# Kernel optimization log

Measured on AMD Instinct MI355X. Metric: run time of the kernel, lower is better.

## Reference

```python
import jax, jax.numpy as jnp
import numpy as np

N_NODES = 100000
N_EDGES = 1600000
NUM_FEAT = 128
HIDDEN = 64
NUM_OUT = 21


def gcn_conv(x, src, dst, norm, W, b, n):
    # PyG GCNConv: h = x @ W (no bias in lin); aggregate normalized messages; add bias.
    h = x @ W  # [N, out]
    msg = h[src] * norm[:, None]  # gather + scale, [E+N, out]
    out = jax.ops.segment_sum(msg, dst, num_segments=n)  # scatter-add, [N, out]
    return out + b


def gcn_norm(edge_index, n, dtype):
    # Add self-loops, compute symmetric normalization deg^-1/2[src]*deg^-1/2[dst].
    loop = jnp.arange(n, dtype=edge_index.dtype)
    src = jnp.concatenate([edge_index[0], loop])
    dst = jnp.concatenate([edge_index[1], loop])
    deg = jax.ops.segment_sum(jnp.ones_like(dst, dtype=dtype), dst, num_segments=n)
    dinv = jnp.where(deg > 0, deg ** -0.5, 0.0).astype(dtype)
    norm = dinv[src] * dinv[dst]
    return src, dst, norm


def setup_inputs() -> dict:
    key = jax.random.key(0)
    k1, k2, k3, k4, k5 = jax.random.split(key, 5)
    x = jax.random.normal(k1, (N_NODES, NUM_FEAT), dtype=jnp.float32)
    edge_index = jax.random.randint(k2, (2, N_EDGES), 0, N_NODES, dtype=jnp.int64)
    s1 = 1.0 / np.sqrt(NUM_FEAT)
    s2 = 1.0 / np.sqrt(HIDDEN)
    W1 = jax.random.uniform(k3, (NUM_FEAT, HIDDEN), jnp.float32, -s1, s1)
    b1 = jnp.zeros((HIDDEN,), jnp.float32)
    W2 = jax.random.uniform(k4, (HIDDEN, NUM_OUT), jnp.float32, -s2, s2)
    b2 = jnp.zeros((NUM_OUT,), jnp.float32)
    return {"x": x, "edge_index": edge_index, "W1": W1, "b1": b1, "W2": W2, "b2": b2}


def reference(x, edge_index, W1, b1, W2, b2):
    n = x.shape[0]
    src, dst, norm = gcn_norm(edge_index, n, x.dtype)
    h = gcn_conv(x, src, dst, norm, W1, b1, n)
    h = jax.nn.relu(h)
    out = gcn_conv(h, src, dst, norm, W2, b2, n)
    return out
```

## Files before the change

### kernel.cpp

```cpp
#include <hip/hip_runtime.h>

#define NFEAT 128
#define NHID  64
#define NOUT  21
#define BSH   7
#define BCAP  8192
#define CHUNK 4096
#define EPT   (CHUNK/256)
#define PADI  16
#define NBUKMAX 1024

typedef unsigned int uint;
typedef unsigned short ushort_t;

typedef __bf16 bf16_t;
typedef bf16_t bf16x8 __attribute__((ext_vector_type(8)));
typedef float  f32x4  __attribute__((ext_vector_type(4)));

__device__ inline uint packbf2(float a, float b) {
    uint ua = __float_as_uint(a), ub = __float_as_uint(b);
    ua = (ua + 0x7FFFu + ((ua >> 16) & 1u)) >> 16;
    ub = (ub + 0x7FFFu + ((ub >> 16) & 1u)) >> 16;
    return ua | (ub << 16);
}
__device__ inline float bflo(uint v) { return __uint_as_float(v << 16); }
__device__ inline float bfhi(uint v) { return __uint_as_float(v & 0xffff0000u); }


__global__ __launch_bounds__(256) void k_lsort(const int* __restrict__ src, const int* __restrict__ dst,
                                               uint* __restrict__ ebuf, int* __restrict__ tab,
                                               int* __restrict__ gcnt, int E, int nbuk) {
    __shared__ int  lcnt[NBUKMAX + 1];
    __shared__ int  lsum[256];
    __shared__ uint lsorted[CHUNK];
    int c = blockIdx.x, tid = threadIdx.x;
    int base = c * CHUNK;
    int ccnt = min(CHUNK, E - base);

    for (int j = tid; j <= nbuk; j += 256) lcnt[j] = 0;
    __syncthreads();

    int  buk[EPT];
    uint rec[EPT];
#pragma unroll
    for (int k = 0; k < EPT; ++k) {
        int e = base + k * 256 + tid;
        if (e < E) {
            int d = dst[e];
            buk[k] = d >> BSH;
            rec[k] = ((uint)(d & ((1 << BSH) - 1)) << 17) | (uint)src[e];
            atomicAdd(&lcnt[buk[k]], 1);
        }
    }
    __syncthreads();

    int g = (nbuk + 255) / 256;
    int j0 = tid * g;
    int s = 0;
    for (int j = 0; j < g; ++j) { int idx = j0 + j; if (idx < nbuk) s += lcnt[idx]; }
    lsum[tid] = s;
    __syncthreads();
    for (int off = 1; off < 256; off <<= 1) {
        int t = (tid >= off) ? lsum[tid - off] : 0;
        __syncthreads();
        lsum[tid] += t;
        __syncthreads();
    }
    int run = lsum[tid] - s;
    for (int j = 0; j < g; ++j) {
        int idx = j0 + j;
        if (idx < nbuk) { int cv = lcnt[idx]; lcnt[idx] = run; run += cv; }
    }
    __syncthreads();
    if (tid == 0) lcnt[nbuk] = ccnt;
    __syncthreads();

    for (int j = tid; j < nbuk; j += 256) {
        int st = lcnt[j];
        tab[(size_t)c * (nbuk + 1) + j] = st;
        int cj = lcnt[j + 1] - st;
        if (cj) atomicAdd(&gcnt[j * PADI], cj);
    }
    if (tid == 0) tab[(size_t)c * (nbuk + 1) + nbuk] = ccnt;
    __syncthreads();

#pragma unroll
    for (int k = 0; k < EPT; ++k) {
        int e = base + k * 256 + tid;
        if (e < E) {
            int pos = atomicAdd(&lcnt[buk[k]], 1);
            lsorted[pos] = rec[k];
        }
    }
    __syncthreads();
    for (int i = tid; i < ccnt; i += 256) ebuf[base + i] = lsorted[i];
}


__global__ __launch_bounds__(256) void k_bscan(const int* __restrict__ gcnt, int* __restrict__ bbase,
                                               int* __restrict__ rowptr, int nbuk, int N, int E) {
    __shared__ int lv[NBUKMAX];
    __shared__ int lsum[256];
    int tid = threadIdx.x;
    int g = (nbuk + 255) / 256;
    int j0 = tid * g;
    int s = 0;
    for (int j = 0; j < g; ++j) {
        int idx = j0 + j;
        int v = (idx < nbuk) ? gcnt[idx * PADI] : 0;
        if (idx < nbuk) lv[idx] = v;
        s += v;
    }
    lsum[tid] = s;
    __syncthreads();
    for (int off = 1; off < 256; off <<= 1) {
        int t = (tid >= off) ? lsum[tid - off] : 0;
        __syncthreads();
        lsum[tid] += t;
        __syncthreads();
    }
    int run = lsum[tid] - s;
    for (int j = 0; j < g; ++j) {
        int idx = j0 + j;
        if (idx < nbuk) { bbase[idx] = run; run += lv[idx]; }
    }
    if (tid == 0) rowptr[N] = E;
}


__global__ __launch_bounds__(256) void k_bsort2(const uint* __restrict__ ebuf, const int* __restrict__ tab,
                                                const int* __restrict__ bbase_, const int* __restrict__ gcnt,
                                                int* __restrict__ rowptr, float* __restrict__ dinv,
                                                int* __restrict__ esrc, int nchunk, int nbuk, int N) {
    __shared__ int  ncnt[128];
    __shared__ int  sc[128];
    __shared__ int  lcur[128];
    __shared__ uint stash[BCAP];
    __shared__ int  lpos;
    int b = blockIdx.x, tid = threadIdx.x;
    int nb0 = b << BSH;
    int bb = bbase_[b];
    int cnt_b = gcnt[b * PADI];
    bool fits = (cnt_b <= BCAP);

    if (tid < 128) ncnt[tid] = 0;
    if (tid == 0) lpos = 0;
    __syncthreads();

    for (int c = tid; c < nchunk; c += 256) {
        const int* trow = tab + (size_t)c * (nbuk + 1);
        int s0 = trow[b], e0 = trow[b + 1];
        int len = e0 - s0;
        if (len <= 0) continue;
        const uint* pb = ebuf + (size_t)c * CHUNK;
        if (fits) {
            int pos = atomicAdd(&lpos, len);
            for (int i = 0; i < len; ++i) {
                uint r = pb[s0 + i];
                stash[pos + i] = r;
                atomicAdd(&ncnt[r >> 17], 1);
            }
        } else {
            for (int i = 0; i < len; ++i) atomicAdd(&ncnt[pb[s0 + i] >> 17], 1);
        }
    }
    __syncthreads();

    int v = (tid < 128) ? ncnt[tid] : 0;
    if (tid < 128) sc[tid] = v;
    __syncthreads();
    for (int off = 1; off < 128; off <<= 1) {
        int t = (tid >= off && tid < 128) ? sc[tid - off] : 0;
        __syncthreads();
        if (tid < 128) sc[tid] += t;
        __syncthreads();
    }
    if (tid < 128) {
        int excl = sc[tid] - v;
        int node = nb0 + tid;
        if (node < N) {
            rowptr[node] = bb + excl;
            dinv[node] = rsqrtf((float)(v + 1));
        }
        lcur[tid] = bb + excl;
    }
    __syncthreads();

    if (fits) {
        for (int i = tid; i < cnt_b; i += 256) {
            uint r = stash[i];
            int pos = atomicAdd(&lcur[r >> 17], 1);
            esrc[pos] = (int)(r & 0x1FFFFu);
        }
    } else {
        for (int c = tid; c < nchunk; c += 256) {
            const int* trow = tab + (size_t)c * (nbuk + 1);
            int s0 = trow[b], e0 = trow[b + 1];
            const uint* pb = ebuf + (size_t)c * CHUNK;
            for (int i = s0; i < e0; ++i) {
                uint r = pb[i];
                int pos = atomicAdd(&lcur[r >> 17], 1);
                esrc[pos] = (int)(r & 0x1FFFFu);
            }
        }
    }
}


__global__ __launch_bounds__(256) void k_count(const int* __restrict__ dst, int* cnt, int E) {
    int e = blockIdx.x * 256 + threadIdx.x;
    if (e < E) atomicAdd(&cnt[dst[e]], 1);
}

__global__ __launch_bounds__(256) void k_scan1(const int* __restrict__ cnt, int* __restrict__ rowptr,
                                               int* __restrict__ bsum, float* __restrict__ dinv, int N) {
    __shared__ int sh[256];
    int tid = threadIdx.x;
    int base = blockIdx.x * 1024 + tid * 4;
    int v[4]; int s = 0;
#pragma unroll
    for (int j = 0; j < 4; ++j) {
        v[j] = (base + j < N) ? cnt[base + j] : 0;
        if (base + j < N) dinv[base + j] = rsqrtf((float)(v[j] + 1));
        s += v[j];
    }
    sh[tid] = s; __syncthreads();
    for (int off = 1; off < 256; off <<= 1) {
        int t = (tid >= off) ? sh[tid - off] : 0;
        __syncthreads();
        sh[tid] += t;
        __syncthreads();
    }
    int run = sh[tid] - s;
#pragma unroll
    for (int j = 0; j < 4; ++j) { if (base + j < N) rowptr[base + j] = run; run += v[j]; }
    if (tid == 255) bsum[blockIdx.x] = sh[255];
}

__global__ __launch_bounds__(128) void k_scan2(int* bsum, int nb) {
    __shared__ int sh[128];
    int tid = threadIdx.x;
    int v = (tid < nb) ? bsum[tid] : 0;
    sh[tid] = v; __syncthreads();
    for (int off = 1; off < 128; off <<= 1) {
        int t = (tid >= off) ? sh[tid - off] : 0;
        __syncthreads();
        sh[tid] += t;
        __syncthreads();
    }
    if (tid < nb) bsum[tid] = sh[tid] - v;
}

__global__ __launch_bounds__(256) void k_scan3(int* __restrict__ rowptr, int* __restrict__ fill,
                                               const int* __restrict__ bsum, int N, int E) {
    int tid = threadIdx.x;
    int base = blockIdx.x * 1024 + tid * 4;
    int add = bsum[blockIdx.x];
#pragma unroll
    for (int j = 0; j < 4; ++j) {
        int idx = base + j;
        if (idx < N) {
            int r = rowptr[idx] + add;
            rowptr[idx] = r;
            fill[idx] = r;
        }
    }
    if (blockIdx.x == 0 && tid == 0) rowptr[N] = E;
}

__global__ __launch_bounds__(256) void k_scatter_direct(const int* __restrict__ src, const int* __restrict__ dst,
                                                        int* __restrict__ fill, int* __restrict__ esrc, int E) {
    int e = blockIdx.x * 256 + threadIdx.x;
    if (e >= E) return;
    int pos = atomicAdd(&fill[dst[e]], 1);
    esrc[pos] = src[e];
}


__global__ __launch_bounds__(256) void k_gemm1(const float* __restrict__ x, const float* __restrict__ W1,
                                               const float* __restrict__ dinv, uint* __restrict__ hb, int N) {
    __shared__ ushort_t xs[64 * 136];
    __shared__ ushort_t ws[64 * 136];
    int tid = threadIdx.x;
    int r0 = blockIdx.x * 64;

    {
        int col = tid & 63;
        int kb = (tid >> 6) * 32;
#pragma unroll
        for (int kk = 0; kk < 32; kk += 2) {
            float a = W1[(size_t)(kb + kk) * NHID + col];
            float b = W1[(size_t)(kb + kk + 1) * NHID + col];
            *(uint*)&ws[col * 136 + kb + kk] = packbf2(a, b);
        }
    }
    {
        int row = tid >> 2;
        int q = tid & 3;
        int grow = r0 + row;
        uint buf[16];
        if (grow < N) {
            const float* xr = x + (size_t)grow * NFEAT + q * 32;
#pragma unroll
            for (int j = 0; j < 8; ++j) {
                float4 v = *(const float4*)&xr[j * 4];
                buf[2 * j]     = packbf2(v.x, v.y);
                buf[2 * j + 1] = packbf2(v.z, v.w);
            }
        } else {
#pragma unroll
            for (int j = 0; j < 16; ++j) buf[j] = 0u;
        }
        uint* d = (uint*)&xs[row * 136 + q * 32];
#pragma unroll
        for (int j = 0; j < 4; ++j)
            ((uint4*)d)[j] = make_uint4(buf[4 * j], buf[4 * j + 1], buf[4 * j + 2], buf[4 * j + 3]);
    }
    __syncthreads();

    int lane = tid & 63;
    int wrow = (tid >> 6) * 16;
    int lrow = lane & 15;
    int lk   = (lane >> 4) * 8;

    f32x4 acc[4];
#pragma unroll
    for (int nt = 0; nt < 4; ++nt) acc[nt] = (f32x4){0.f, 0.f, 0.f, 0.f};

#pragma unroll
    for (int kq = 0; kq < 4; ++kq) {
        int k0 = kq * 32;
        bf16x8 a = *(const bf16x8*)&xs[(wrow + lrow) * 136 + k0 + lk];
#pragma unroll
        for (int nt = 0; nt < 4; ++nt) {
            bf16x8 b = *(const bf16x8*)&ws[(nt * 16 + lrow) * 136 + k0 + lk];
            acc[nt] = __builtin_amdgcn_mfma_f32_16x16x32_bf16(a, b, acc[nt], 0, 0, 0);
        }
    }

    int orow0 = (lane >> 4) * 4;
    float dvv[4];
#pragma unroll
    for (int r = 0; r < 4; ++r) {
        int grow = r0 + wrow + orow0 + r;
        dvv[r] = (grow < N) ? dinv[grow] : 0.f;
    }
    ushort_t* hbs = (ushort_t*)hb;
#pragma unroll
    for (int nt = 0; nt < 4; ++nt) {
#pragma unroll
        for (int r = 0; r < 4; ++r) {
            int grow = r0 + wrow + orow0 + r;
            if (grow < N) {
                uint pb = packbf2(acc[nt][r] * dvv[r], 0.f);
                hbs[(size_t)grow * 64 + nt * 16 + lrow] = (ushort_t)(pb & 0xffffu);
            }
        }
    }
}


__global__ __launch_bounds__(256) void k_agg1(const int* __restrict__ rowptr, const int* __restrict__ esrc,
                                              const uint* __restrict__ hb, const float* __restrict__ dinv,
                                              const float* __restrict__ b1, float* __restrict__ o1, int N) {
    int tid = threadIdx.x;
    int node = blockIdx.x * 4 + (tid >> 6);
    if (node >= N) return;
    int lane = tid & 63;
    int half = lane >> 5;
    int c = lane & 31;
    uint sv = hb[(size_t)node * 32 + c];
    float ax = half ? 0.f : bflo(sv);
    float ay = half ? 0.f : bfhi(sv);
    int beg = rowptr[node], end = rowptr[node + 1];
    int i = beg + half;
    for (; i + 14 < end; i += 16) {
        int s0 = esrc[i], s1 = esrc[i + 2], s2 = esrc[i + 4], s3 = esrc[i + 6];
        int s4 = esrc[i + 8], s5 = esrc[i + 10], s6 = esrc[i + 12], s7 = esrc[i + 14];
        uint v0 = hb[(size_t)s0 * 32 + c];
        uint v1 = hb[(size_t)s1 * 32 + c];
        uint v2 = hb[(size_t)s2 * 32 + c];
        uint v3 = hb[(size_t)s3 * 32 + c];
        uint v4 = hb[(size_t)s4 * 32 + c];
        uint v5 = hb[(size_t)s5 * 32 + c];
        uint v6 = hb[(size_t)s6 * 32 + c];
        uint v7 = hb[(size_t)s7 * 32 + c];
        ax += bflo(v0) + bflo(v1);
        ay += bfhi(v0) + bfhi(v1);
        ax += bflo(v2) + bflo(v3);
        ay += bfhi(v2) + bfhi(v3);
        ax += bflo(v4) + bflo(v5);
        ay += bfhi(v4) + bfhi(v5);
        ax += bflo(v6) + bflo(v7);
        ay += bfhi(v6) + bfhi(v7);
    }
    for (; i + 6 < end; i += 8) {
        int s0 = esrc[i], s1 = esrc[i + 2], s2 = esrc[i + 4], s3 = esrc[i + 6];
        uint v0 = hb[(size_t)s0 * 32 + c];
        uint v1 = hb[(size_t)s1 * 32 + c];
        uint v2 = hb[(size_t)s2 * 32 + c];
        uint v3 = hb[(size_t)s3 * 32 + c];
        ax += bflo(v0) + bflo(v1);
        ay += bfhi(v0) + bfhi(v1);
        ax += bflo(v2) + bflo(v3);
        ay += bfhi(v2) + bfhi(v3);
    }
    for (; i < end; i += 2) {
        uint v = hb[(size_t)esrc[i] * 32 + c];
        ax += bflo(v); ay += bfhi(v);
    }
    ax += __shfl_xor(ax, 32);
    ay += __shfl_xor(ay, 32);
    if (!half) {
        float dv = dinv[node];
        float2 bv = ((const float2*)b1)[c];
        float2 r;
        r.x = fmaxf(fmaf(ax, dv, bv.x), 0.f);
        r.y = fmaxf(fmaf(ay, dv, bv.y), 0.f);
        ((float2*)(o1 + (size_t)node * NHID))[c] = r;
    }
}


__global__ __launch_bounds__(128) void k_gemm2(const float* __restrict__ o1, const float* __restrict__ W2,
                                               const float* __restrict__ dinv, uint* __restrict__ h2b, int N) {
    __shared__ float rs[128 * 65];
    __shared__ float Ws[NHID * NOUT];
    int tid = threadIdx.x;
    for (int i = tid; i < NHID * NOUT; i += 128) Ws[i] = W2[i];
    int base = blockIdx.x * 128;
#pragma unroll
    for (int i = 0; i < 16; ++i) {
        int idx = tid + i * 128;
        int row = idx >> 4;
        int f4 = (idx & 15) * 4;
        int grow = base + row;
        float4 v = make_float4(0.f, 0.f, 0.f, 0.f);
        if (grow < N) v = *(const float4*)&o1[(size_t)grow * NHID + f4];
        float* d = &rs[row * 65 + f4];
        d[0] = v.x; d[1] = v.y; d[2] = v.z; d[3] = v.w;
    }
    __syncthreads();
    int row = base + tid;
    if (row >= N) return;
    float acc[NOUT];
#pragma unroll
    for (int j = 0; j < NOUT; ++j) acc[j] = 0.f;
    for (int k = 0; k < NHID; ++k) {
        float av = rs[tid * 65 + k];
#pragma unroll
        for (int j = 0; j < NOUT; ++j) acc[j] = fmaf(av, Ws[k * NOUT + j], acc[j]);
    }
    float dv = dinv[row];
    uint up[16];
#pragma unroll
    for (int j = 0; j < 10; ++j) up[j] = packbf2(acc[2 * j] * dv, acc[2 * j + 1] * dv);
    up[10] = packbf2(acc[20] * dv, 0.f);
#pragma unroll
    for (int j = 11; j < 16; ++j) up[j] = 0u;
    uint* hr = h2b + (size_t)row * 16;
    ((uint4*)hr)[0] = make_uint4(up[0], up[1], up[2], up[3]);
    ((uint4*)hr)[1] = make_uint4(up[4], up[5], up[6], up[7]);
    ((uint4*)hr)[2] = make_uint4(up[8], up[9], up[10], up[11]);
    ((uint4*)hr)[3] = make_uint4(up[12], up[13], up[14], up[15]);
}


__global__ __launch_bounds__(256) void k_agg2(const int* __restrict__ rowptr, const int* __restrict__ esrc,
                                              const uint* __restrict__ h2b, const float* __restrict__ dinv,
                                              const float* __restrict__ b2, float* __restrict__ out, int N) {
    int tid = threadIdx.x;
    int node = blockIdx.x * 64 + (tid >> 2);
    if (node >= N) return;
    int q = tid & 3;
    uint4 sv = *((const uint4*)(h2b + (size_t)node * 16) + q);
    float a0 = bflo(sv.x), a1 = bfhi(sv.x), a2 = bflo(sv.y), a3 = bfhi(sv.y);
    float a4 = bflo(sv.z), a5 = bfhi(sv.z), a6 = bflo(sv.w), a7 = bfhi(sv.w);
    int beg = rowptr[node], end = rowptr[node + 1];
    int i = beg;
    for (; i + 3 < end; i += 4) {
        int s0 = esrc[i], s1 = esrc[i + 1], s2 = esrc[i + 2], s3 = esrc[i + 3];
        uint4 v0 = *((const uint4*)(h2b + (size_t)s0 * 16) + q);
        uint4 v1 = *((const uint4*)(h2b + (size_t)s1 * 16) + q);
        uint4 v2 = *((const uint4*)(h2b + (size_t)s2 * 16) + q);
        uint4 v3 = *((const uint4*)(h2b + (size_t)s3 * 16) + q);
        a0 += bflo(v0.x) + bflo(v1.x);
        a1 += bfhi(v0.x) + bfhi(v1.x);
        a2 += bflo(v0.y) + bflo(v1.y);
        a3 += bfhi(v0.y) + bfhi(v1.y);
        a4 += bflo(v0.z) + bflo(v1.z);
        a5 += bfhi(v0.z) + bfhi(v1.z);
        a6 += bflo(v0.w) + bflo(v1.w);
        a7 += bfhi(v0.w) + bfhi(v1.w);
        a0 += bflo(v2.x) + bflo(v3.x);
        a1 += bfhi(v2.x) + bfhi(v3.x);
        a2 += bflo(v2.y) + bflo(v3.y);
        a3 += bfhi(v2.y) + bfhi(v3.y);
        a4 += bflo(v2.z) + bflo(v3.z);
        a5 += bfhi(v2.z) + bfhi(v3.z);
        a6 += bflo(v2.w) + bflo(v3.w);
        a7 += bfhi(v2.w) + bfhi(v3.w);
    }
    for (; i < end; ++i) {
        uint4 v0 = *((const uint4*)(h2b + (size_t)esrc[i] * 16) + q);
        a0 += bflo(v0.x); a1 += bfhi(v0.x);
        a2 += bflo(v0.y); a3 += bfhi(v0.y);
        a4 += bflo(v0.z); a5 += bfhi(v0.z);
        a6 += bflo(v0.w); a7 += bfhi(v0.w);
    }
    float dv = dinv[node];
    float* orow = out + (size_t)node * NOUT;
    int col = q * 8;
    float av[8] = {a0, a1, a2, a3, a4, a5, a6, a7};
#pragma unroll
    for (int j = 0; j < 8; ++j)
        if (col + j < NOUT) orow[col + j] = fmaf(dv, av[j], b2[col + j]);
}


extern "C" void kernel_launch(void* const* d_in, const int* in_sizes, int n_in,
                              void* d_out, int out_size, void* d_ws, size_t ws_size,
                              hipStream_t stream) {
    const float* x  = (const float*)d_in[0];
    const int*   ei = (const int*)d_in[1];
    const float* W1 = (const float*)d_in[2];
    const float* b1 = (const float*)d_in[3];
    const float* W2 = (const float*)d_in[4];
    const float* b2 = (const float*)d_in[5];
    float* out = (float*)d_out;

    int N = in_sizes[0] / NFEAT;
    int E = in_sizes[1] / 2;
    const int* src = ei;
    const int* dst = ei + E;
    int NBUK = (N + (1 << BSH) - 1) >> BSH;
    int NCHUNK = (E + CHUNK - 1) / CHUNK;

    char* p = (char*)d_ws;
    auto alloc = [&](size_t bytes) { void* r = (void*)p; p += (bytes + 255) & ~(size_t)255; return r; };
    int*   rowptr = (int*)alloc((size_t)(N + 1) * 4);
    int*   gcnt   = (int*)alloc((size_t)NBUK * PADI * 4);
    int*   bbase  = (int*)alloc((size_t)NBUK * 4);
    int*   tab    = (int*)alloc((size_t)NCHUNK * (NBUK + 1) * 4);
    uint*  ebuf   = (uint*)alloc((size_t)E * 4);
    int*   esrc   = (int*)alloc((size_t)E * 4);
    float* dinv   = (float*)alloc((size_t)N * 4);
    uint*  hb     = (uint*)alloc((size_t)N * 32 * 4);
    float* o1     = (float*)alloc((size_t)N * NHID * 4);
    uint*  h2b    = (uint*)alloc((size_t)N * 16 * 4);
    int*   cnt    = (int*)alloc((size_t)N * 4);
    int*   fill   = (int*)alloc((size_t)N * 4);
    int*   bsum   = (int*)alloc(128 * 4);

    const int B = 256;

    if (N <= (1 << 17)) {
        hipMemsetAsync(gcnt, 0, (size_t)NBUK * PADI * 4, stream);
        k_lsort <<<NCHUNK, 256, 0, stream>>>(src, dst, ebuf, tab, gcnt, E, NBUK);
        k_bscan <<<1, 256, 0, stream>>>(gcnt, bbase, rowptr, NBUK, N, E);
        k_bsort2<<<NBUK, 256, 0, stream>>>(ebuf, tab, bbase, gcnt, rowptr, dinv, esrc, NCHUNK, NBUK, N);
    } else {
        int nb = (N + 1023) / 1024;
        hipMemsetAsync(cnt, 0, (size_t)N * 4, stream);
        k_count <<<(E + B - 1) / B, B, 0, stream>>>(dst, cnt, E);
        k_scan1 <<<nb, 256, 0, stream>>>(cnt, rowptr, bsum, dinv, N);
        k_scan2 <<<1, 128, 0, stream>>>(bsum, nb);
        k_scan3 <<<nb, 256, 0, stream>>>(rowptr, fill, bsum, N, E);
        k_scatter_direct<<<(E + B - 1) / B, B, 0, stream>>>(src, dst, fill, esrc, E);
    }

    k_gemm1 <<<(N + 63) / 64, 256, 0, stream>>>(x, W1, dinv, hb, N);
    k_agg1  <<<(N + 3) / 4, 256, 0, stream>>>(rowptr, esrc, hb, dinv, b1, o1, N);
    k_gemm2 <<<(N + 127) / 128, 128, 0, stream>>>(o1, W2, dinv, h2b, N);
    k_agg2  <<<(N + 63) / 64, 256, 0, stream>>>(rowptr, esrc, h2b, dinv, b2, out, N);
}
```

Baseline: 177.2 us.

## Fuse layer-2 linear transform into layer-1 aggregation kernel

Merges the second GEMM into the first aggregation kernel. Each wavefront keeps its aggregated hidden row in shared memory, multiplies it by W2 held in LDS using 21 lanes, and writes the packed bf16 h2 row directly. This removes the o1 intermediate buffer (a 25.6MB write and read) and one kernel launch. In exchange, every block of 4 nodes reloads W2 (about 5KB) into LDS, and the small per-node GEMV leaves most lanes idle.

```diff
diff --git a/kernel.cpp b/kernel.cpp
--- a/kernel.cpp
+++ b/kernel.cpp
@@ -360,11 +360,18 @@
 }
 
 
-__global__ __launch_bounds__(256) void k_agg1(const int* __restrict__ rowptr, const int* __restrict__ esrc,
-                                              const uint* __restrict__ hb, const float* __restrict__ dinv,
-                                              const float* __restrict__ b1, float* __restrict__ o1, int N) {
-    int tid = threadIdx.x;
-    int node = blockIdx.x * 4 + (tid >> 6);
+__global__ __launch_bounds__(256) void k_agg1f(const int* __restrict__ rowptr, const int* __restrict__ esrc,
+                                               const uint* __restrict__ hb, const float* __restrict__ dinv,
+                                               const float* __restrict__ b1, const float* __restrict__ W2,
+                                               uint* __restrict__ h2b, int N) {
+    __shared__ float W2s[NHID * NOUT];
+    __shared__ float o1s[4][NHID];
+    int tid = threadIdx.x;
+    for (int i = tid; i < NHID * NOUT; i += 256) W2s[i] = W2[i];
+    __syncthreads();
+
+    int wid = tid >> 6;
+    int node = blockIdx.x * 4 + wid;
     if (node >= N) return;
     int lane = tid & 63;
     int half = lane >> 5;
@@ -411,58 +418,27 @@
     }
     ax += __shfl_xor(ax, 32);
     ay += __shfl_xor(ay, 32);
+    float dv = dinv[node];
     if (!half) {
-        float dv = dinv[node];
         float2 bv = ((const float2*)b1)[c];
         float2 r;
         r.x = fmaxf(fmaf(ax, dv, bv.x), 0.f);
         r.y = fmaxf(fmaf(ay, dv, bv.y), 0.f);
-        ((float2*)(o1 + (size_t)node * NHID))[c] = r;
-    }
-}
-
-
-__global__ __launch_bounds__(128) void k_gemm2(const float* __restrict__ o1, const float* __restrict__ W2,
-                                               const float* __restrict__ dinv, uint* __restrict__ h2b, int N) {
-    __shared__ float rs[128 * 65];
-    __shared__ float Ws[NHID * NOUT];
-    int tid = threadIdx.x;
-    for (int i = tid; i < NHID * NOUT; i += 128) Ws[i] = W2[i];
-    int base = blockIdx.x * 128;
-#pragma unroll
-    for (int i = 0; i < 16; ++i) {
-        int idx = tid + i * 128;
-        int row = idx >> 4;
-        int f4 = (idx & 15) * 4;
-        int grow = base + row;
-        float4 v = make_float4(0.f, 0.f, 0.f, 0.f);
-        if (grow < N) v = *(const float4*)&o1[(size_t)grow * NHID + f4];
-        float* d = &rs[row * 65 + f4];
-        d[0] = v.x; d[1] = v.y; d[2] = v.z; d[3] = v.w;
-    }
-    __syncthreads();
-    int row = base + tid;
-    if (row >= N) return;
-    float acc[NOUT];
-#pragma unroll
-    for (int j = 0; j < NOUT; ++j) acc[j] = 0.f;
-    for (int k = 0; k < NHID; ++k) {
-        float av = rs[tid * 65 + k];
-#pragma unroll
-        for (int j = 0; j < NOUT; ++j) acc[j] = fmaf(av, Ws[k * NOUT + j], acc[j]);
-    }
-    float dv = dinv[row];
-    uint up[16];
-#pragma unroll
-    for (int j = 0; j < 10; ++j) up[j] = packbf2(acc[2 * j] * dv, acc[2 * j + 1] * dv);
-    up[10] = packbf2(acc[20] * dv, 0.f);
-#pragma unroll
-    for (int j = 11; j < 16; ++j) up[j] = 0u;
-    uint* hr = h2b + (size_t)row * 16;
-    ((uint4*)hr)[0] = make_uint4(up[0], up[1], up[2], up[3]);
-    ((uint4*)hr)[1] = make_uint4(up[4], up[5], up[6], up[7]);
-    ((uint4*)hr)[2] = make_uint4(up[8], up[9], up[10], up[11]);
-    ((uint4*)hr)[3] = make_uint4(up[12], up[13], up[14], up[15]);
+        *(float2*)&o1s[wid][2 * c] = r;
+    }
+    __threadfence_block();
+
+    float h2v = 0.f;
+    if (lane < NOUT) {
+        const float* orow = o1s[wid];
+        float accj = 0.f;
+#pragma unroll 8
+        for (int k = 0; k < NHID; ++k) accj = fmaf(orow[k], W2s[k * NOUT + lane], accj);
+        h2v = accj * dv;
+    }
+    float lo = __shfl(h2v, 2 * (lane & 15));
+    float hi = __shfl(h2v, 2 * (lane & 15) + 1);
+    if (lane < 16) h2b[(size_t)node * 16 + lane] = packbf2(lo, hi);
 }
 
 
@@ -546,7 +522,6 @@
     int*   esrc   = (int*)alloc((size_t)E * 4);
     float* dinv   = (float*)alloc((size_t)N * 4);
     uint*  hb     = (uint*)alloc((size_t)N * 32 * 4);
-    float* o1     = (float*)alloc((size_t)N * NHID * 4);
     uint*  h2b    = (uint*)alloc((size_t)N * 16 * 4);
     int*   cnt    = (int*)alloc((size_t)N * 4);
     int*   fill   = (int*)alloc((size_t)N * 4);
@@ -570,7 +545,6 @@
     }
 
     k_gemm1 <<<(N + 63) / 64, 256, 0, stream>>>(x, W1, dinv, hb, N);
-    k_agg1  <<<(N + 3) / 4, 256, 0, stream>>>(rowptr, esrc, hb, dinv, b1, o1, N);
-    k_gemm2 <<<(N + 127) / 128, 128, 0, stream>>>(o1, W2, dinv, h2b, N);
+    k_agg1f <<<(N + 3) / 4, 256, 0, stream>>>(rowptr, esrc, hb, dinv, b1, W2, h2b, N);
     k_agg2  <<<(N + 63) / 64, 256, 0, stream>>>(rowptr, esrc, h2b, dinv, b2, out, N);
 }
```

Result: slower. 182.5 us (+3.0%).
